# Kernel tuning notes

Measured on AMD Instinct MI355X. Metric: run time of the kernel, lower is better.

Reference implementation:

```python
import jax, jax.numpy as jnp
import numpy as np
import math

PHI = (1 + math.sqrt(5)) / 2
PI = math.pi
B, L, D, V, NL, PAD = 2, 384, 256, 32000, 3, 0


def _ln(t, eps):
    mu = t.mean(-1, keepdims=True)
    var = ((t - mu) ** 2).mean(-1, keepdims=True)
    return (t - mu) / jnp.sqrt(var + eps)


def setup_inputs() -> dict:
    key = jax.random.key(0)
    ks = jax.random.split(key, 8)
    return {
        'x': jax.random.randint(ks[0], (B, L), 0, V, dtype=jnp.int32),
        'emb_real': jax.random.normal(ks[1], (V, D), jnp.float32) * 0.02,
        'emb_imag': jax.random.normal(ks[2], (V, D), jnp.float32) * 0.02,
        'layer_phases': jax.random.normal(ks[3], (NL, D), jnp.float32) * 0.02,
        'interference_weights': jax.random.normal(ks[4], (NL, D), jnp.float32) * 0.02,
        'energy_levels': jnp.linspace(0.0, 1.0, D).astype(jnp.float32),
        'excitation_factor': jnp.ones((1,), jnp.float32) * 0.1,
        'phase_preservation': jnp.ones((NL, D), jnp.float32) * 0.1,
        'coherence_factor': jnp.ones((NL, 1), jnp.float32) * 0.1,
        'W_attn': jax.random.normal(ks[5], (NL, D, D), jnp.float32) * 0.02,
        'out_w': jax.random.normal(ks[6], (2 * D, V), jnp.float32) * 0.02,
        'out_b': jnp.zeros((V,), jnp.float32),
    }


def _forward(x, emb_real, emb_imag, layer_phases, interference_weights,
             energy_levels, excitation_factor, phase_preservation,
             coherence_factor, W_attn, out_w, out_b):
    re = emb_real[x] * 0.1                      # [B,L,D]
    _unused_imag = emb_imag[x] * 0.1            # imag embedding unused downstream (as in original)
    # ---- EnhancedDynamicPhaseSpace ----
    fr = jnp.zeros_like(re)
    fi = jnp.zeros_like(re)
    for i in range(NL):
        pa = jnp.tanh(layer_phases[i]) * PI * PHI      # [D]
        r = _ln(re * jnp.cos(pa), 1e-8)
        im = _ln(re * jnp.sin(pa), 1e-8)
        w = jnp.tanh(interference_weights[i])
        r = r * w
        im = im * w
        a = 2.0 * PI * i / NL
        ca, sa = math.cos(a), math.sin(a)
        fr = fr + r * ca - im * sa
        fi = fi + r * sa + im * ca
    amp = jnp.sqrt(fr * fr + fi * fi + 1e-8)
    coll = (amp < 0.1).astype(re.dtype)
    exc = jnp.exp(energy_levels) * excitation_factor   # [D]
    fr = fr + coll * exc
    fi = fi + coll * exc
    nrm = jnp.sqrt(fr * fr + fi * fi + 1e-8)
    real = jnp.clip(fr / nrm, -1.0, 1.0)
    imag = jnp.clip(fi / nrm, -1.0, 1.0)
    # ---- 3 QuantumStatePreservingAttention layers ----
    pad_mask = (x == PAD)                               # [B,L]
    scale = D ** (-0.5)
    for i in range(NL):
        # q/k/v LayerNorms are parameter-free here and q=k=v, so one norm each
        nr = _ln(real, 1e-5)
        ni = _ln(imag, 1e-5)
        ph = jnp.arctan2(ni + 1e-8, nr + 1e-8)          # [B,L,D]
        pdiff = ph[:, :, None, :] - ph[:, None, :, :]   # [B,L,L,D]
        interf = jnp.cos(pdiff)                         # [B,L,L,D]
        # mean over last dim of (interf @ W) == interf . row-means of W (same math)
        w_mean = W_attn[i].mean(axis=1)                 # [D]
        scores = jnp.einsum('blmd,d->blm', interf, w_mean) * scale
        scores = jnp.where(pad_mask[:, None, :], -jnp.inf, scores)
        attn = jnp.clip(jax.nn.softmax(scores, axis=-1), 1e-6, 1.0)
        out_r = jnp.einsum('blm,bmd->bld', attn, nr)
        out_i = jnp.einsum('blm,bmd->bld', attn, ni)
        coh = interf.mean(axis=(-1, -2))                # [B,L]
        cf = jax.nn.sigmoid(coherence_factor[i]) * coh[..., None]
        phase = jnp.arctan2(out_i + 1e-8, out_r + 1e-8)
        pres = jax.nn.sigmoid(phase_preservation[i]) * cf
        pr = out_r * jnp.cos(phase * pres)
        pim = out_i * jnp.sin(phase * pres)
        real = jnp.clip(_ln(real + 0.01 * pr, 1e-8), -1.0, 1.0)
        _dead = _ln(imag + 0.01 * pim, 1e-8)            # computed then overwritten in original
        imag = real                                     # original bug: imag = clamp(real, -1, 1)
    combined = _ln(jnp.concatenate([real, imag], axis=-1), 1e-5)
    logits = jnp.clip((combined @ out_w + out_b) * 0.1, -10.0, 10.0)
    return logits


def reference(x, emb_real, emb_imag, layer_phases, interference_weights,
              energy_levels, excitation_factor, phase_preservation,
              coherence_factor, W_attn, out_w, out_b):
    return _forward(x, emb_real, emb_imag, layer_phases, interference_weights,
                    energy_levels, excitation_factor, phase_preservation,
                    coherence_factor, W_attn, out_w, out_b)
```

## Files before the change

kernel.cpp:

```cpp
#include <hip/hip_runtime.h>
#include <hip/hip_bf16.h>
#include <math.h>

typedef __hip_bfloat16 bf16;
typedef __bf16 bf16x8 __attribute__((ext_vector_type(8)));
typedef float f32x4 __attribute__((ext_vector_type(4)));

#define NTOK 768
#define SEQ  384
#define DDIM 256
#define VOC  32000

__device__ __forceinline__ float bf2f(bf16 v) { return __bfloat162float(v); }

__device__ __forceinline__ bool probe_bf(const void* energy) {
    return ((const unsigned short*)energy)[1] != 0;
}
__device__ __forceinline__ float ldin(const void* p, long i, bool bf) {
    return bf ? bf2f(((const bf16*)p)[i]) : ((const float*)p)[i];
}

__device__ __forceinline__ float blk_sum256(float v, float* red) {
    #pragma unroll
    for (int o = 32; o > 0; o >>= 1) v += __shfl_down(v, o, 64);
    int w = threadIdx.x >> 6;
    __syncthreads();
    if ((threadIdx.x & 63) == 0) red[w] = v;
    __syncthreads();
    return red[0] + red[1] + red[2] + red[3];
}

__device__ __forceinline__ void np_emit(int t, int d, float nrv, float niv, bool dual,
                                        const float* __restrict__ wm,
                                        float* __restrict__ nrO, float* __restrict__ niO,
                                        float* __restrict__ Co, float* __restrict__ So,
                                        bf16* __restrict__ ASh, bf16* __restrict__ ASl,
                                        bf16* __restrict__ BSh, bf16* __restrict__ BSl)
{
    float ph = atan2f(niv + 1e-8f, nrv + 1e-8f);
    float Cv = cosf(ph), Sv = sinf(ph);
    long idx = (long)t * DDIM + d;
    nrO[idx] = nrv;
    if (dual) niO[idx] = niv;
    Co[idx] = Cv;
    So[idx] = Sv;
    float wv = wm[d];
    float aC = Cv * wv, aS = Sv * wv;
    long o0 = (long)t * 512 + d, o1 = o0 + 256;
    bf16 h;
    h = __float2bfloat16(aC); ASh[o0] = h; ASl[o0] = __float2bfloat16(aC - bf2f(h));
    h = __float2bfloat16(aS); ASh[o1] = h; ASl[o1] = __float2bfloat16(aS - bf2f(h));
    h = __float2bfloat16(Cv); BSh[o0] = h; BSl[o0] = __float2bfloat16(Cv - bf2f(h));
    h = __float2bfloat16(Sv); BSh[o1] = h; BSl[o1] = __float2bfloat16(Sv - bf2f(h));
}

__global__ __launch_bounds__(256)
void phase_kernel(const int* __restrict__ x, const void* __restrict__ emb,
                  const void* __restrict__ lph, const void* __restrict__ iw,
                  const void* __restrict__ energy, const void* __restrict__ excf,
                  const float* __restrict__ wm0,
                  float* __restrict__ realO,
                  float* __restrict__ nrO, float* __restrict__ niO,
                  float* __restrict__ Co, float* __restrict__ So,
                  bf16* __restrict__ ASh, bf16* __restrict__ ASl,
                  bf16* __restrict__ BSh, bf16* __restrict__ BSl)
{
    __shared__ float red[4];
    bool bf = probe_bf(energy);
    int t = blockIdx.x, d = threadIdx.x;
    int tok = x[t];
    float re = ldin(emb, (long)tok * DDIM + d, bf) * 0.1f;
    float fr = 0.f, fi = 0.f;
    const float ca[3] = {1.0f, -0.5f, -0.5f};
    const float sa[3] = {0.0f, 0.86602540378443864676f, -0.86602540378443864676f};
    #pragma unroll
    for (int i = 0; i < 3; ++i) {
        float pa = tanhf(ldin(lph, i * DDIM + d, bf)) * 3.14159265358979323846f;
        pa = pa * 1.61803398874989484820f;
        float vr = re * cosf(pa);
        float vi = re * sinf(pa);
        float mu = blk_sum256(vr, red) * (1.f / 256.f);
        float dv = vr - mu;
        float var = blk_sum256(dv * dv, red) * (1.f / 256.f);
        float r = dv / sqrtf(var + 1e-8f);
        mu = blk_sum256(vi, red) * (1.f / 256.f);
        float di = vi - mu;
        var = blk_sum256(di * di, red) * (1.f / 256.f);
        float im = di / sqrtf(var + 1e-8f);
        float w = tanhf(ldin(iw, i * DDIM + d, bf));
        r *= w; im *= w;
        fr = fr + r * ca[i] - im * sa[i];
        fi = fi + r * sa[i] + im * ca[i];
    }
    float amp = sqrtf(fr * fr + fi * fi + 1e-8f);
    float ex = expf(ldin(energy, d, bf)) * ldin(excf, 0, bf);
    if (amp < 0.1f) { fr += ex; fi += ex; }
    float nrm = sqrtf(fr * fr + fi * fi + 1e-8f);
    float rr = fminf(fmaxf(fr / nrm, -1.f), 1.f);
    float ii = fminf(fmaxf(fi / nrm, -1.f), 1.f);
    realO[t * DDIM + d] = rr;
    float mu = blk_sum256(rr, red) * (1.f / 256.f);
    float dv = rr - mu;
    float var = blk_sum256(dv * dv, red) * (1.f / 256.f);
    float nrv = dv / sqrtf(var + 1e-5f);
    mu = blk_sum256(ii, red) * (1.f / 256.f);
    float di = ii - mu;
    var = blk_sum256(di * di, red) * (1.f / 256.f);
    float niv = di / sqrtf(var + 1e-5f);
    np_emit(t, d, nrv, niv, true, wm0, nrO, niO, Co, So, ASh, ASl, BSh, BSl);
}

__global__ __launch_bounds__(256)
void wmean_kernel(const void* __restrict__ W, const void* __restrict__ energy,
                  float* __restrict__ wmAll)
{
    bool bf = probe_bf(energy);
    int row = blockIdx.x * 4 + (threadIdx.x >> 6);
    int lane = threadIdx.x & 63;
    long base = (long)row * DDIM + lane * 4;
    float s = 0.f;
    #pragma unroll
    for (int j = 0; j < 4; ++j) s += ldin(W, base + j, bf);
    #pragma unroll
    for (int o = 32; o > 0; o >>= 1) s += __shfl_down(s, o, 64);
    if (lane == 0) wmAll[row] = s * (1.f / 256.f) * 0.0625f;
}

__global__ __launch_bounds__(256)
void sums_kernel(const float* __restrict__ C, const float* __restrict__ S,
                 float* __restrict__ Cp, float* __restrict__ Sp)
{
    int c = blockIdx.x, b = blockIdx.y, d = threadIdx.x;
    float cs = 0.f, ss = 0.f;
    int base = (b * SEQ + c * 16) * DDIM + d;
    #pragma unroll
    for (int m = 0; m < 16; ++m) { cs += C[base + m * DDIM]; ss += S[base + m * DDIM]; }
    Cp[(b * 24 + c) * DDIM + d] = cs;
    Sp[(b * 24 + c) * DDIM + d] = ss;
}

__global__ __launch_bounds__(256)
void transpose_kernel(const float* __restrict__ nr, const float* __restrict__ ni,
                      bf16* __restrict__ nrTh, bf16* __restrict__ nrTl,
                      bf16* __restrict__ niTh, bf16* __restrict__ niTl, int dual)
{
    __shared__ float tr[64][65], ti[64][65];
    int m0 = blockIdx.x * 64, d0 = blockIdx.y * 64, b = blockIdx.z;
    int c = threadIdx.x & 63, rr = threadIdx.x >> 6;
    #pragma unroll
    for (int i = 0; i < 16; ++i) {
        int r = i * 4 + rr;
        tr[r][c] = nr[(b * SEQ + m0 + r) * DDIM + d0 + c];
        if (dual) ti[r][c] = ni[(b * SEQ + m0 + r) * DDIM + d0 + c];
    }
    __syncthreads();
    #pragma unroll
    for (int i = 0; i < 16; ++i) {
        int dd = i * 4 + rr;
        long o = (long)(b * DDIM + d0 + dd) * SEQ + m0 + c;
        float vr = tr[c][dd];
        bf16 h;
        h = __float2bfloat16(vr); nrTh[o] = h; nrTl[o] = __float2bfloat16(vr - bf2f(h));
        if (dual) {
            float vi = ti[c][dd];
            h = __float2bfloat16(vi); niTh[o] = h; niTl[o] = __float2bfloat16(vi - bf2f(h));
        }
    }
}

__device__ __forceinline__ void gload_lds16(const bf16* g, bf16* l) {
    __builtin_amdgcn_global_load_lds(
        (const __attribute__((address_space(1))) unsigned int*)g,
        (__attribute__((address_space(3))) unsigned int*)l,
        16, 0, 0);
}

__global__ __launch_bounds__(256, 4)
void scores_mfma(const bf16* __restrict__ ASh, const bf16* __restrict__ ASl,
                 const bf16* __restrict__ BSh, const bf16* __restrict__ BSl,
                 float* __restrict__ scores)
{
    __shared__ bf16 ldsA[2][64 * 64];
    __shared__ bf16 ldsB[2][32 * 64];
    int l0 = blockIdx.x * 64, m0 = blockIdx.y * 32, b = blockIdx.z;
    int tid = threadIdx.x, lane = tid & 63, wid = tid >> 6;
    int wr = wid >> 1, wc = wid & 1;
    int lrow = lane >> 3;
    int cbs  = (lane & 7) ^ lrow;

    const bf16* srcA = (wid == 1 ? ASl : ASh) + (size_t)(b * SEQ + l0) * 512;
    const bf16* srcB = (wid == 3 ? BSl : BSh) + (size_t)(b * SEQ + m0) * 512;

    f32x4 acc[2] = {};

    for (int k0 = 0; k0 < 512; k0 += 64) {
        if (wid < 2) {
            bf16* ld = &ldsA[wid][0];
            #pragma unroll
            for (int q = 0; q < 8; ++q)
                gload_lds16(srcA + (size_t)(q * 8 + lrow) * 512 + k0 + cbs * 8, ld + q * 512);
        } else {
            bf16* ld = &ldsB[wid - 2][0];
            #pragma unroll
            for (int q = 0; q < 4; ++q)
                gload_lds16(srcB + (size_t)(q * 8 + lrow) * 512 + k0 + cbs * 8, ld + q * 512);
        }
        __syncthreads();
        #pragma unroll
        for (int ks = 0; ks < 2; ++ks) {
            int cb = ks * 64 + (lane >> 4) * 16;
            int rowb = wc * 16 + (lane & 15);
            int offb = rowb * 128 + (cb ^ ((rowb & 7) << 4));
            bf16x8 bh = *(const bf16x8*)((const char*)&ldsB[0][0] + offb);
            bf16x8 bl = *(const bf16x8*)((const char*)&ldsB[1][0] + offb);
            #pragma unroll
            for (int fm = 0; fm < 2; ++fm) {
                int rowa = wr * 32 + fm * 16 + (lane & 15);
                int offa = rowa * 128 + (cb ^ ((rowa & 7) << 4));
                bf16x8 ah = *(const bf16x8*)((const char*)&ldsA[0][0] + offa);
                bf16x8 al = *(const bf16x8*)((const char*)&ldsA[1][0] + offa);
                acc[fm] = __builtin_amdgcn_mfma_f32_16x16x32_bf16(ah, bh, acc[fm], 0, 0, 0);
                acc[fm] = __builtin_amdgcn_mfma_f32_16x16x32_bf16(ah, bl, acc[fm], 0, 0, 0);
                acc[fm] = __builtin_amdgcn_mfma_f32_16x16x32_bf16(al, bh, acc[fm], 0, 0, 0);
            }
        }
        __syncthreads();
    }

    int mm = m0 + wc * 16 + (lane & 15);
    #pragma unroll
    for (int fm = 0; fm < 2; ++fm) {
        int lbase = l0 + wr * 32 + fm * 16 + (lane >> 4) * 4;
        #pragma unroll
        for (int i = 0; i < 4; ++i)
            scores[(size_t)(b * SEQ + lbase + i) * SEQ + mm] = acc[fm][i];
    }
}

__global__ __launch_bounds__(384)
void softmax_kernel(const float* __restrict__ scores, const int* __restrict__ x,
                    bf16* __restrict__ Ph, bf16* __restrict__ Pl)
{
    __shared__ float red[6];
    int row = blockIdx.x;
    int b = row / SEQ;
    int m = threadIdx.x;
    float s = scores[row * SEQ + m];
    if (x[b * SEQ + m] == 0) s = -__builtin_inff();
    float v = s;
    #pragma unroll
    for (int o = 32; o > 0; o >>= 1) v = fmaxf(v, __shfl_down(v, o, 64));
    if ((threadIdx.x & 63) == 0) red[threadIdx.x >> 6] = v;
    __syncthreads();
    float mx = red[0];
    #pragma unroll
    for (int i = 1; i < 6; ++i) mx = fmaxf(mx, red[i]);
    float p = expf(s - mx);
    __syncthreads();
    v = p;
    #pragma unroll
    for (int o = 32; o > 0; o >>= 1) v += __shfl_down(v, o, 64);
    if ((threadIdx.x & 63) == 0) red[threadIdx.x >> 6] = v;
    __syncthreads();
    float sum = red[0] + red[1] + red[2] + red[3] + red[4] + red[5];
    float pv = p / sum;
    pv = fminf(fmaxf(pv, 1e-6f), 1.0f);
    bf16 h = __float2bfloat16(pv);
    Ph[(size_t)row * SEQ + m] = h;
    Pl[(size_t)row * SEQ + m] = __float2bfloat16(pv - bf2f(h));
}

__global__ __launch_bounds__(256, 4)
void outgemm_mfma(const bf16* __restrict__ Ph, const bf16* __restrict__ Pl,
                  const bf16* __restrict__ nrTh, const bf16* __restrict__ nrTl,
                  const bf16* __restrict__ niTh, const bf16* __restrict__ niTl,
                  float* __restrict__ outr, float* __restrict__ outi, int dual)
{
    __shared__ bf16 ldsA[2][64 * 64];
    __shared__ bf16 ldsB[4][32 * 64];
    int l0 = blockIdx.x * 64, d0 = blockIdx.y * 32, b = blockIdx.z;
    int tid = threadIdx.x, lane = tid & 63, wid = tid >> 6;
    int wr = wid >> 1, wc = wid & 1;
    int lrow = lane >> 3, cbs = (lane & 7) ^ lrow;

    const bf16* sA  = (wid == 0 ? Ph : Pl) + (size_t)(b * SEQ + l0) * SEQ;
    const bf16* sB1 = (wid == 2 ? nrTh : nrTl) + (size_t)(b * DDIM + d0) * SEQ;
    const bf16* sB2 = (wid == 2 ? niTh : niTl) + (size_t)(b * DDIM + d0) * SEQ;

    f32x4 accr[2] = {}, acci[2] = {};

    for (int k0 = 0; k0 < SEQ; k0 += 64) {
        if (wid < 2) {
            bf16* ld = &ldsA[wid][0];
            #pragma unroll
            for (int q = 0; q < 8; ++q)
                gload_lds16(sA + (size_t)(q * 8 + lrow) * SEQ + k0 + cbs * 8, ld + q * 512);
        } else {
            bf16* l1 = &ldsB[wid - 2][0];
            #pragma unroll
            for (int q = 0; q < 4; ++q)
                gload_lds16(sB1 + (size_t)(q * 8 + lrow) * SEQ + k0 + cbs * 8, l1 + q * 512);
            if (dual) {
                bf16* l2 = &ldsB[wid][0];
                #pragma unroll
                for (int q = 0; q < 4; ++q)
                    gload_lds16(sB2 + (size_t)(q * 8 + lrow) * SEQ + k0 + cbs * 8, l2 + q * 512);
            }
        }
        __syncthreads();
        #pragma unroll
        for (int ks = 0; ks < 2; ++ks) {
            int cb = ks * 64 + (lane >> 4) * 16;
            int rowb = wc * 16 + (lane & 15);
            int offb = rowb * 128 + (cb ^ ((rowb & 7) << 4));
            bf16x8 brh = *(const bf16x8*)((const char*)&ldsB[0][0] + offb);
            bf16x8 brl = *(const bf16x8*)((const char*)&ldsB[1][0] + offb);
            #pragma unroll
            for (int fm = 0; fm < 2; ++fm) {
                int rowa = wr * 32 + fm * 16 + (lane & 15);
                int offa = rowa * 128 + (cb ^ ((rowa & 7) << 4));
                bf16x8 ah = *(const bf16x8*)((const char*)&ldsA[0][0] + offa);
                bf16x8 al = *(const bf16x8*)((const char*)&ldsA[1][0] + offa);
                accr[fm] = __builtin_amdgcn_mfma_f32_16x16x32_bf16(ah, brh, accr[fm], 0, 0, 0);
                accr[fm] = __builtin_amdgcn_mfma_f32_16x16x32_bf16(ah, brl, accr[fm], 0, 0, 0);
                accr[fm] = __builtin_amdgcn_mfma_f32_16x16x32_bf16(al, brh, accr[fm], 0, 0, 0);
            }
            if (dual) {
                bf16x8 bih = *(const bf16x8*)((const char*)&ldsB[2][0] + offb);
                bf16x8 bil = *(const bf16x8*)((const char*)&ldsB[3][0] + offb);
                #pragma unroll
                for (int fm = 0; fm < 2; ++fm) {
                    int rowa = wr * 32 + fm * 16 + (lane & 15);
                    int offa = rowa * 128 + (cb ^ ((rowa & 7) << 4));
                    bf16x8 ah = *(const bf16x8*)((const char*)&ldsA[0][0] + offa);
                    bf16x8 al = *(const bf16x8*)((const char*)&ldsA[1][0] + offa);
                    acci[fm] = __builtin_amdgcn_mfma_f32_16x16x32_bf16(ah, bih, acci[fm], 0, 0, 0);
                    acci[fm] = __builtin_amdgcn_mfma_f32_16x16x32_bf16(ah, bil, acci[fm], 0, 0, 0);
                    acci[fm] = __builtin_amdgcn_mfma_f32_16x16x32_bf16(al, bih, acci[fm], 0, 0, 0);
                }
            }
        }
        __syncthreads();
    }

    int d = d0 + wc * 16 + (lane & 15);
    #pragma unroll
    for (int fm = 0; fm < 2; ++fm) {
        int lb = l0 + wr * 32 + fm * 16 + (lane >> 4) * 4;
        #pragma unroll
        for (int i = 0; i < 4; ++i) {
            size_t idx = (size_t)(b * SEQ + lb + i) * DDIM + d;
            outr[idx] = accr[fm][i];
            if (dual) outi[idx] = acci[fm][i];
        }
    }
}

__global__ __launch_bounds__(256)
void update_kernel(float* __restrict__ realA,
                   const float* __restrict__ outr, const float* __restrict__ outi,
                   const float* __restrict__ C, const float* __restrict__ S,
                   const float* __restrict__ Cp, const float* __restrict__ Sp,
                   const void* __restrict__ pp, const void* __restrict__ cfac,
                   const void* __restrict__ energy, int layer, int mode,
                   const float* __restrict__ wmNext,
                   float* __restrict__ nrO, float* __restrict__ Co, float* __restrict__ So,
                   bf16* __restrict__ ASh, bf16* __restrict__ ASl,
                   bf16* __restrict__ BSh, bf16* __restrict__ BSl,
                   bf16* __restrict__ Ah, bf16* __restrict__ Al)
{
    __shared__ float red[4];
    bool bf = probe_bf(energy);
    int t = blockIdx.x, d = threadIdx.x;
    int b = t / SEQ;
    long idx = (long)t * DDIM + d;
    float cs = 0.f, ss = 0.f;
    #pragma unroll
    for (int c = 0; c < 24; ++c) {
        cs += Cp[(b * 24 + c) * DDIM + d];
        ss += Sp[(b * 24 + c) * DDIM + d];
    }
    float dotv = C[idx] * cs + S[idx] * ss;
    float coh = blk_sum256(dotv, red) * (1.0f / (384.f * 256.f));
    float cf = (1.f / (1.f + expf(-ldin(cfac, layer, bf)))) * coh;
    float orr = outr[idx], oii = outi[idx];
    float phase = atan2f(oii + 1e-8f, orr + 1e-8f);
    float pres = (1.f / (1.f + expf(-ldin(pp, layer * DDIM + d, bf)))) * cf;
    float pr = orr * cosf(phase * pres);
    float v = realA[idx] + 0.01f * pr;
    float mu = blk_sum256(v, red) * (1.f / 256.f);
    float dv = v - mu;
    float var = blk_sum256(dv * dv, red) * (1.f / 256.f);
    float nv = dv / sqrtf(var + 1e-8f);
    nv = fminf(fmaxf(nv, -1.f), 1.f);
    realA[idx] = nv;
    float mu2 = blk_sum256(nv, red) * (1.f / 256.f);
    float dv2 = nv - mu2;
    float var2 = blk_sum256(dv2 * dv2, red) * (1.f / 256.f);
    float nn = dv2 / sqrtf(var2 + 1e-5f);
    if (mode == 0) {
        np_emit(t, d, nn, nn, false, wmNext, nrO, nullptr, Co, So, ASh, ASl, BSh, BSl);
    } else {
        bf16 h = __float2bfloat16(nn);
        Ah[idx] = h;
        Al[idx] = __float2bfloat16(nn - bf2f(h));
    }
}


__global__ __launch_bounds__(256)
void fold_kernel(const void* __restrict__ W, const void* __restrict__ energy,
                 bf16* __restrict__ Bh, bf16* __restrict__ Bl)
{
    __shared__ float tile[64][65];
    bool bf = probe_bf(energy);
    int v0 = blockIdx.x * 64, d0 = blockIdx.y * 64;
    int c = threadIdx.x & 63, rr = threadIdx.x >> 6;
    #pragma unroll
    for (int i = 0; i < 16; ++i) {
        int r = i * 4 + rr;
        long i1 = (long)(d0 + r) * VOC + v0 + c;
        long i2 = (long)(d0 + r + 256) * VOC + v0 + c;
        tile[r][c] = ldin(W, i1, bf) + ldin(W, i2, bf);
    }
    __syncthreads();
    int d = threadIdx.x & 63, vv = threadIdx.x >> 6;
    #pragma unroll
    for (int i = 0; i < 16; ++i) {
        int v = i * 4 + vv;
        float s = tile[d][v];
        bf16 h = __float2bfloat16(s);
        long o = (long)(v0 + v) * DDIM + d0 + d;
        Bh[o] = h;
        Bl[o] = __float2bfloat16(s - __bfloat162float(h));
    }
}

__global__ __launch_bounds__(512, 4)
void vocab_gemm(const bf16* __restrict__ Ah, const bf16* __restrict__ Al,
                const bf16* __restrict__ Bh, const bf16* __restrict__ Bl,
                const void* __restrict__ bias, const void* __restrict__ energy,
                void* __restrict__ out)
{
    __shared__ bf16 lds[4][128 * 64];
    bool bf = probe_bf(energy);
    int flat = blockIdx.x + blockIdx.y * 6;
    int xcd = flat & 7, bidx = flat >> 3;
    int swz = (xcd < 4) ? xcd * 188 + bidx : 752 + (xcd - 4) * 187 + bidx;
    int m0 = (swz % 6) * 128, n0 = (swz / 6) * 128;
    int tid = threadIdx.x, lane = tid & 63, wid = tid >> 6;
    int wm = wid >> 2, wn = wid & 3;
    int arr = wid >> 1, half = wid & 1;

    const bf16* src;
    if      (arr == 0) src = Ah + (size_t)m0 * DDIM;
    else if (arr == 1) src = Al + (size_t)m0 * DDIM;
    else if (arr == 2) src = Bh + (size_t)n0 * DDIM;
    else               src = Bl + (size_t)n0 * DDIM;
    src += (size_t)half * 64 * DDIM;
    bf16* ldst = &lds[arr][half * 64 * 64];
    int lrow = lane >> 3;
    int cbs  = (lane & 7) ^ lrow;

    f32x4 acc[4][2] = {};

    for (int k0 = 0; k0 < DDIM; k0 += 64) {
        #pragma unroll
        for (int q = 0; q < 8; ++q) {
            const bf16* g = src + (size_t)(q * 8 + lrow) * DDIM + k0 + cbs * 8;
            gload_lds16(g, ldst + q * 512);
        }
        __syncthreads();

        #pragma unroll
        for (int ks = 0; ks < 2; ++ks) {
            int cb = ks * 64 + (lane >> 4) * 16;
            bf16x8 bhf[2], blf[2];
            #pragma unroll
            for (int fn = 0; fn < 2; ++fn) {
                int row = wn * 32 + fn * 16 + (lane & 15);
                int off = row * 128 + (cb ^ ((row & 7) << 4));
                bhf[fn] = *(const bf16x8*)((const char*)&lds[2][0] + off);
                blf[fn] = *(const bf16x8*)((const char*)&lds[3][0] + off);
            }
            #pragma unroll
            for (int fm = 0; fm < 4; ++fm) {
                int row = wm * 64 + fm * 16 + (lane & 15);
                int off = row * 128 + (cb ^ ((row & 7) << 4));
                bf16x8 ah = *(const bf16x8*)((const char*)&lds[0][0] + off);
                bf16x8 al = *(const bf16x8*)((const char*)&lds[1][0] + off);
                #pragma unroll
                for (int fn = 0; fn < 2; ++fn) {
                    acc[fm][fn] = __builtin_amdgcn_mfma_f32_16x16x32_bf16(ah, bhf[fn], acc[fm][fn], 0, 0, 0);
                    acc[fm][fn] = __builtin_amdgcn_mfma_f32_16x16x32_bf16(ah, blf[fn], acc[fm][fn], 0, 0, 0);
                    acc[fm][fn] = __builtin_amdgcn_mfma_f32_16x16x32_bf16(al, bhf[fn], acc[fm][fn], 0, 0, 0);
                }
            }
        }
        __syncthreads();
    }

    #pragma unroll
    for (int fn = 0; fn < 2; ++fn) {
        int n = n0 + wn * 32 + fn * 16 + (lane & 15);
        float bv = ldin(bias, n, bf);
        #pragma unroll
        for (int fm = 0; fm < 4; ++fm) {
            int mbase = m0 + wm * 64 + fm * 16 + (lane >> 4) * 4;
            #pragma unroll
            for (int i = 0; i < 4; ++i) {
                float lg = (acc[fm][fn][i] + bv) * 0.1f;
                lg = fminf(fmaxf(lg, -10.f), 10.f);
                size_t idx = (size_t)(mbase + i) * VOC + n;
                if (bf) ((bf16*)out)[idx] = __float2bfloat16(lg);
                else    ((float*)out)[idx] = lg;
            }
        }
    }
}

extern "C" void kernel_launch(void* const* d_in, const int* in_sizes, int n_in,
                              void* d_out, int out_size, void* d_ws, size_t ws_size,
                              hipStream_t stream) {
    (void)in_sizes; (void)n_in; (void)out_size; (void)ws_size;
    const int*  x        = (const int*)d_in[0];
    const void* emb_real = d_in[1];
    const void* lph      = d_in[3];
    const void* iw       = d_in[4];
    const void* energy   = d_in[5];
    const void* excf     = d_in[6];
    const void* pp       = d_in[7];
    const void* cfac     = d_in[8];
    const void* Wattn    = d_in[9];
    const void* out_w    = d_in[10];
    const void* out_b    = d_in[11];

    float* ws = (float*)d_ws;
    const int TD = NTOK * DDIM;
    float* realA = ws;
    float* nr    = realA + TD;
    float* ni    = nr + TD;
    float* Cc    = ni + TD;
    float* Ss    = Cc + TD;
    float* outr  = Ss + TD;
    float* outi  = outr + TD;
    float* attn  = outi + TD;
    float* Cp    = attn + 2 * SEQ * SEQ;
    float* Sp    = Cp + 48 * DDIM;
    float* wmAll = Sp + 48 * DDIM;
    bf16* Ah  = (bf16*)(wmAll + 768);
    bf16* Al  = Ah + (size_t)NTOK * DDIM;
    bf16* Wth = Al + (size_t)NTOK * DDIM;
    bf16* Wtl = Wth + (size_t)VOC * DDIM;
    bf16* ASh = Wtl + (size_t)VOC * DDIM;
    bf16* ASl = ASh + (size_t)NTOK * 512;
    bf16* BSh = ASl + (size_t)NTOK * 512;
    bf16* BSl = BSh + (size_t)NTOK * 512;
    bf16* Phb = BSl + (size_t)NTOK * 512;
    bf16* Plb = Phb + (size_t)NTOK * SEQ;
    bf16* nrTh = Plb + (size_t)NTOK * SEQ;
    bf16* nrTl = nrTh + (size_t)NTOK * DDIM;
    bf16* niTh = nrTl + (size_t)NTOK * DDIM;
    bf16* niTl = niTh + (size_t)NTOK * DDIM;

    fold_kernel<<<dim3(VOC / 64, DDIM / 64), 256, 0, stream>>>(out_w, energy, Wth, Wtl);
    wmean_kernel<<<192, 256, 0, stream>>>(Wattn, energy, wmAll);

    phase_kernel<<<NTOK, 256, 0, stream>>>(x, emb_real, lph, iw, energy, excf, wmAll,
                                           realA, nr, ni, Cc, Ss, ASh, ASl, BSh, BSl);
    for (int layer = 0; layer < 3; ++layer) {
        int dual = (layer == 0);
        sums_kernel<<<dim3(24, 2), 256, 0, stream>>>(Cc, Ss, Cp, Sp);
        transpose_kernel<<<dim3(6, 4, 2), 256, 0, stream>>>(nr, ni, nrTh, nrTl, niTh, niTl, dual);
        scores_mfma<<<dim3(6, 12, 2), 256, 0, stream>>>(ASh, ASl, BSh, BSl, attn);
        softmax_kernel<<<NTOK, 384, 0, stream>>>(attn, x, Phb, Plb);
        outgemm_mfma<<<dim3(6, 8, 2), 256, 0, stream>>>(Phb, Plb, nrTh, nrTl, niTh, niTl,
                                                        outr, outi, dual);
        update_kernel<<<NTOK, 256, 0, stream>>>(realA, outr, dual ? outi : outr, Cc, Ss,
                                                Cp, Sp, pp, cfac, energy, layer,
                                                (layer < 2) ? 0 : 1,
                                                wmAll + (layer + 1 < 3 ? (layer + 1) * DDIM : 0),
                                                nr, Cc, Ss, ASh, ASl, BSh, BSl, Ah, Al);
    }
    vocab_gemm<<<dim3(6, VOC / 128), 512, 0, stream>>>(Ah, Al, Wth, Wtl, out_b, energy, (void*)d_out);
}
```

Before: 367.7 us.

## Fuse per-layer attention kernels into one cooperative persistent kernel with grid syncs

Replaces the 18 per-layer kernel launches (sums, transpose, scores, softmax, outgemm, update) with a single cooperative kernel. It walks work units in a grid-stride loop and separates the phases with grid-wide syncs. Scores and outgemm tiles shrink to 32x32 per block so more blocks share the work, and sums/transpose/scores run in the same phase. The goal is to remove launch overhead and inter-kernel gaps. The cost is grid-sync latency and smaller tiles with less reuse, and the old multi-kernel path stays as a fallback if the cooperative launch fails.

```diff
diff --git a/kernel.cpp b/kernel.cpp
--- a/kernel.cpp
+++ b/kernel.cpp
@@ -1,4 +1,5 @@
 #include <hip/hip_runtime.h>
+#include <hip/hip_cooperative_groups.h>
 #include <hip/hip_bf16.h>
 #include <math.h>
 
@@ -20,14 +21,21 @@
     return bf ? bf2f(((const bf16*)p)[i]) : ((const float*)p)[i];
 }
 
-__device__ __forceinline__ float blk_sum256(float v, float* red) {
+__device__ __forceinline__ float blk_sum256s(float v, float* red) {
     #pragma unroll
     for (int o = 32; o > 0; o >>= 1) v += __shfl_down(v, o, 64);
-    int w = threadIdx.x >> 6;
     __syncthreads();
-    if ((threadIdx.x & 63) == 0) red[w] = v;
+    if ((threadIdx.x & 63) == 0) red[threadIdx.x >> 6] = v;
     __syncthreads();
     return red[0] + red[1] + red[2] + red[3];
+}
+__device__ __forceinline__ float blk_max256s(float v, float* red) {
+    #pragma unroll
+    for (int o = 32; o > 0; o >>= 1) v = fmaxf(v, __shfl_down(v, o, 64));
+    __syncthreads();
+    if ((threadIdx.x & 63) == 0) red[threadIdx.x >> 6] = v;
+    __syncthreads();
+    return fmaxf(fmaxf(red[0], red[1]), fmaxf(red[2], red[3]));
 }
 
 __device__ __forceinline__ void np_emit(int t, int d, float nrv, float niv, bool dual,
@@ -54,6 +62,349 @@
     h = __float2bfloat16(Sv); BSh[o1] = h; BSl[o1] = __float2bfloat16(Sv - bf2f(h));
 }
 
+__device__ __forceinline__ void gload_lds16(const bf16* g, bf16* l) {
+    __builtin_amdgcn_global_load_lds(
+        (const __attribute__((address_space(1))) unsigned int*)g,
+        (__attribute__((address_space(3))) unsigned int*)l,
+        16, 0, 0);
+}
+
+
+__device__ __forceinline__ void scores_unit(int l0, int m0, int b, char* smem,
+    const bf16* __restrict__ ASh, const bf16* __restrict__ ASl,
+    const bf16* __restrict__ BSh, const bf16* __restrict__ BSl,
+    float* __restrict__ scores)
+{
+    bf16* ldsA0 = (bf16*)smem;
+    bf16* ldsA1 = ldsA0 + 2048;
+    bf16* ldsB0 = ldsA1 + 2048;
+    bf16* ldsB1 = ldsB0 + 2048;
+    int tid = threadIdx.x, lane = tid & 63, wid = tid >> 6;
+    int wr = wid >> 1, wc = wid & 1;
+    int lrow = lane >> 3, cbs = (lane & 7) ^ lrow;
+    const bf16* src = (wid == 0 ? ASh : wid == 1 ? ASl : wid == 2 ? BSh : BSl)
+                      + (size_t)(b * SEQ + (wid < 2 ? l0 : m0)) * 512;
+    bf16* ld = (wid == 0 ? ldsA0 : wid == 1 ? ldsA1 : wid == 2 ? ldsB0 : ldsB1);
+    f32x4 acc = {};
+    for (int k0 = 0; k0 < 512; k0 += 64) {
+        #pragma unroll
+        for (int q = 0; q < 4; ++q)
+            gload_lds16(src + (size_t)(q * 8 + lrow) * 512 + k0 + cbs * 8, ld + q * 512);
+        __syncthreads();
+        #pragma unroll
+        for (int ks = 0; ks < 2; ++ks) {
+            int cb = ks * 64 + (lane >> 4) * 16;
+            int rowb = wc * 16 + (lane & 15);
+            int offb = rowb * 128 + (cb ^ ((rowb & 7) << 4));
+            bf16x8 bh = *(const bf16x8*)((const char*)ldsB0 + offb);
+            bf16x8 bl = *(const bf16x8*)((const char*)ldsB1 + offb);
+            int rowa = wr * 16 + (lane & 15);
+            int offa = rowa * 128 + (cb ^ ((rowa & 7) << 4));
+            bf16x8 ah = *(const bf16x8*)((const char*)ldsA0 + offa);
+            bf16x8 al = *(const bf16x8*)((const char*)ldsA1 + offa);
+            acc = __builtin_amdgcn_mfma_f32_16x16x32_bf16(ah, bh, acc, 0, 0, 0);
+            acc = __builtin_amdgcn_mfma_f32_16x16x32_bf16(ah, bl, acc, 0, 0, 0);
+            acc = __builtin_amdgcn_mfma_f32_16x16x32_bf16(al, bh, acc, 0, 0, 0);
+        }
+        __syncthreads();
+    }
+    int mm = m0 + wc * 16 + (lane & 15);
+    int lbase = l0 + wr * 16 + (lane >> 4) * 4;
+    #pragma unroll
+    for (int i = 0; i < 4; ++i)
+        scores[(size_t)(b * SEQ + lbase + i) * SEQ + mm] = acc[i];
+}
+
+__device__ __forceinline__ void transpose_unit(int m0, int d0, int b, char* smem, int dual,
+    const float* __restrict__ nr, const float* __restrict__ ni,
+    bf16* __restrict__ nrTh, bf16* __restrict__ nrTl,
+    bf16* __restrict__ niTh, bf16* __restrict__ niTl)
+{
+    float* tr = (float*)smem;
+    float* ti = tr + 64 * 65;
+    int c = threadIdx.x & 63, rr = threadIdx.x >> 6;
+    #pragma unroll
+    for (int i = 0; i < 16; ++i) {
+        int r = i * 4 + rr;
+        tr[r * 65 + c] = nr[(b * SEQ + m0 + r) * DDIM + d0 + c];
+        if (dual) ti[r * 65 + c] = ni[(b * SEQ + m0 + r) * DDIM + d0 + c];
+    }
+    __syncthreads();
+    #pragma unroll
+    for (int i = 0; i < 16; ++i) {
+        int dd = i * 4 + rr;
+        long o = (long)(b * DDIM + d0 + dd) * SEQ + m0 + c;
+        float vr = tr[c * 65 + dd];
+        bf16 h;
+        h = __float2bfloat16(vr); nrTh[o] = h; nrTl[o] = __float2bfloat16(vr - bf2f(h));
+        if (dual) {
+            float vi = ti[c * 65 + dd];
+            h = __float2bfloat16(vi); niTh[o] = h; niTl[o] = __float2bfloat16(vi - bf2f(h));
+        }
+    }
+    __syncthreads();
+}
+
+__device__ __forceinline__ void sums_unit(int c, int b,
+    const float* __restrict__ C, const float* __restrict__ S,
+    float* __restrict__ Cp, float* __restrict__ Sp)
+{
+    int d = threadIdx.x;
+    float cs = 0.f, ss = 0.f;
+    int base = (b * SEQ + c * 16) * DDIM + d;
+    #pragma unroll
+    for (int m = 0; m < 16; ++m) { cs += C[base + m * DDIM]; ss += S[base + m * DDIM]; }
+    Cp[(b * 24 + c) * DDIM + d] = cs;
+    Sp[(b * 24 + c) * DDIM + d] = ss;
+}
+
+__device__ __forceinline__ void softmax_unit(int row, float* red,
+    const float* __restrict__ scores, const int* __restrict__ x,
+    bf16* __restrict__ Ph, bf16* __restrict__ Pl)
+{
+    int b = row / SEQ;
+    int tid = threadIdx.x;
+    float s1 = scores[(size_t)row * SEQ + tid];
+    if (x[b * SEQ + tid] == 0) s1 = -__builtin_inff();
+    float s2 = -__builtin_inff();
+    if (tid < 128) {
+        s2 = scores[(size_t)row * SEQ + 256 + tid];
+        if (x[b * SEQ + 256 + tid] == 0) s2 = -__builtin_inff();
+    }
+    float mx = blk_max256s(fmaxf(s1, s2), red);
+    float e1 = expf(s1 - mx);
+    float e2 = (tid < 128) ? expf(s2 - mx) : 0.f;
+    float sum = blk_sum256s(e1 + e2, red);
+    float p1 = fminf(fmaxf(e1 / sum, 1e-6f), 1.0f);
+    bf16 h = __float2bfloat16(p1);
+    Ph[(size_t)row * SEQ + tid] = h;
+    Pl[(size_t)row * SEQ + tid] = __float2bfloat16(p1 - bf2f(h));
+    if (tid < 128) {
+        float p2 = fminf(fmaxf(e2 / sum, 1e-6f), 1.0f);
+        h = __float2bfloat16(p2);
+        Ph[(size_t)row * SEQ + 256 + tid] = h;
+        Pl[(size_t)row * SEQ + 256 + tid] = __float2bfloat16(p2 - bf2f(h));
+    }
+}
+
+__device__ __forceinline__ void outgemm_unit(int l0, int d0, int b, char* smem, int dual,
+    const bf16* __restrict__ Ph, const bf16* __restrict__ Pl,
+    const bf16* __restrict__ nrTh, const bf16* __restrict__ nrTl,
+    const bf16* __restrict__ niTh, const bf16* __restrict__ niTl,
+    float* __restrict__ outr, float* __restrict__ outi)
+{
+    bf16* ldsA0 = (bf16*)smem;
+    bf16* ldsA1 = ldsA0 + 2048;
+    bf16* ldsB0 = ldsA1 + 2048;
+    bf16* ldsB1 = ldsB0 + 2048;
+    bf16* ldsB2 = ldsB1 + 2048;
+    bf16* ldsB3 = ldsB2 + 2048;
+    int tid = threadIdx.x, lane = tid & 63, wid = tid >> 6;
+    int wr = wid >> 1, wc = wid & 1;
+    int lrow = lane >> 3, cbs = (lane & 7) ^ lrow;
+
+    const bf16* sA  = (wid == 0 ? Ph : Pl) + (size_t)(b * SEQ + l0) * SEQ;
+    const bf16* sB1 = (wid == 2 ? nrTh : nrTl) + (size_t)(b * DDIM + d0) * SEQ;
+    const bf16* sB2 = (wid == 2 ? niTh : niTl) + (size_t)(b * DDIM + d0) * SEQ;
+
+    f32x4 accr = {}, acci = {};
+
+    for (int k0 = 0; k0 < SEQ; k0 += 64) {
+        if (wid < 2) {
+            bf16* ld = (wid == 0) ? ldsA0 : ldsA1;
+            #pragma unroll
+            for (int q = 0; q < 4; ++q)
+                gload_lds16(sA + (size_t)(q * 8 + lrow) * SEQ + k0 + cbs * 8, ld + q * 512);
+        } else {
+            bf16* l1 = (wid == 2) ? ldsB0 : ldsB1;
+            #pragma unroll
+            for (int q = 0; q < 4; ++q)
+                gload_lds16(sB1 + (size_t)(q * 8 + lrow) * SEQ + k0 + cbs * 8, l1 + q * 512);
+            if (dual) {
+                bf16* l2 = (wid == 2) ? ldsB2 : ldsB3;
+                #pragma unroll
+                for (int q = 0; q < 4; ++q)
+                    gload_lds16(sB2 + (size_t)(q * 8 + lrow) * SEQ + k0 + cbs * 8, l2 + q * 512);
+            }
+        }
+        __syncthreads();
+        #pragma unroll
+        for (int ks = 0; ks < 2; ++ks) {
+            int cb = ks * 64 + (lane >> 4) * 16;
+            int rowb = wc * 16 + (lane & 15);
+            int offb = rowb * 128 + (cb ^ ((rowb & 7) << 4));
+            int rowa = wr * 16 + (lane & 15);
+            int offa = rowa * 128 + (cb ^ ((rowa & 7) << 4));
+            bf16x8 ah = *(const bf16x8*)((const char*)ldsA0 + offa);
+            bf16x8 al = *(const bf16x8*)((const char*)ldsA1 + offa);
+            bf16x8 brh = *(const bf16x8*)((const char*)ldsB0 + offb);
+            bf16x8 brl = *(const bf16x8*)((const char*)ldsB1 + offb);
+            accr = __builtin_amdgcn_mfma_f32_16x16x32_bf16(ah, brh, accr, 0, 0, 0);
+            accr = __builtin_amdgcn_mfma_f32_16x16x32_bf16(ah, brl, accr, 0, 0, 0);
+            accr = __builtin_amdgcn_mfma_f32_16x16x32_bf16(al, brh, accr, 0, 0, 0);
+            if (dual) {
+                bf16x8 bih = *(const bf16x8*)((const char*)ldsB2 + offb);
+                bf16x8 bil = *(const bf16x8*)((const char*)ldsB3 + offb);
+                acci = __builtin_amdgcn_mfma_f32_16x16x32_bf16(ah, bih, acci, 0, 0, 0);
+                acci = __builtin_amdgcn_mfma_f32_16x16x32_bf16(ah, bil, acci, 0, 0, 0);
+                acci = __builtin_amdgcn_mfma_f32_16x16x32_bf16(al, bih, acci, 0, 0, 0);
+            }
+        }
+        __syncthreads();
+    }
+
+    int d = d0 + wc * 16 + (lane & 15);
+    int lb = l0 + wr * 16 + (lane >> 4) * 4;
+    #pragma unroll
+    for (int i = 0; i < 4; ++i) {
+        size_t idx = (size_t)(b * SEQ + lb + i) * DDIM + d;
+        outr[idx] = accr[i];
+        if (dual) outi[idx] = acci[i];
+    }
+}
+
+__device__ __forceinline__ void update_unit(int t, float* red,
+    float* __restrict__ realA,
+    const float* __restrict__ outr, const float* __restrict__ outi,
+    const float* __restrict__ C, const float* __restrict__ S,
+    const float* __restrict__ Cp, const float* __restrict__ Sp,
+    const void* __restrict__ pp, const void* __restrict__ cfac,
+    const void* __restrict__ energy, int layer, int mode,
+    const float* __restrict__ wmNext,
+    float* __restrict__ nrO, float* __restrict__ Co, float* __restrict__ So,
+    bf16* __restrict__ ASh, bf16* __restrict__ ASl,
+    bf16* __restrict__ BSh, bf16* __restrict__ BSl,
+    bf16* __restrict__ Ah, bf16* __restrict__ Al)
+{
+    bool bf = probe_bf(energy);
+    int d = threadIdx.x;
+    int b = t / SEQ;
+    long idx = (long)t * DDIM + d;
+    float cs = 0.f, ss = 0.f;
+    #pragma unroll
+    for (int c = 0; c < 24; ++c) {
+        cs += Cp[(b * 24 + c) * DDIM + d];
+        ss += Sp[(b * 24 + c) * DDIM + d];
+    }
+    float dotv = C[idx] * cs + S[idx] * ss;
+    float coh = blk_sum256s(dotv, red) * (1.0f / (384.f * 256.f));
+    float cf = (1.f / (1.f + expf(-ldin(cfac, layer, bf)))) * coh;
+    float orr = outr[idx], oii = outi[idx];
+    float phase = atan2f(oii + 1e-8f, orr + 1e-8f);
+    float pres = (1.f / (1.f + expf(-ldin(pp, layer * DDIM + d, bf)))) * cf;
+    float pr = orr * cosf(phase * pres);
+    float v = realA[idx] + 0.01f * pr;
+    float mu = blk_sum256s(v, red) * (1.f / 256.f);
+    float dv = v - mu;
+    float var = blk_sum256s(dv * dv, red) * (1.f / 256.f);
+    float nv = dv / sqrtf(var + 1e-8f);
+    nv = fminf(fmaxf(nv, -1.f), 1.f);
+    realA[idx] = nv;
+    float mu2 = blk_sum256s(nv, red) * (1.f / 256.f);
+    float dv2 = nv - mu2;
+    float var2 = blk_sum256s(dv2 * dv2, red) * (1.f / 256.f);
+    float nn = dv2 / sqrtf(var2 + 1e-5f);
+    if (mode == 0) {
+        np_emit(t, d, nn, nn, false, wmNext, nrO, nullptr, Co, So, ASh, ASl, BSh, BSl);
+    } else {
+        bf16 h = __float2bfloat16(nn);
+        Ah[idx] = h;
+        Al[idx] = __float2bfloat16(nn - bf2f(h));
+    }
+}
+
+struct CoopArgs {
+    const int* x;
+    const void* pp; const void* cfac; const void* energy;
+    float* realA; float* nr; float* ni; float* Cc; float* Ss;
+    float* outr; float* outi; float* attn; float* Cp; float* Sp;
+    const float* wmAll;
+    bf16 *ASh, *ASl, *BSh, *BSl, *Phb, *Plb;
+    bf16 *nrTh, *nrTl, *niTh, *niTl, *Ah, *Al;
+};
+
+__global__ __launch_bounds__(256)
+void coop_layers(CoopArgs a)
+{
+    __shared__ __align__(16) char smem[33280];
+    cooperative_groups::grid_group g = cooperative_groups::this_grid();
+    int bid = blockIdx.x, G = gridDim.x;
+    for (int layer = 0; layer < 3; ++layer) {
+        int dual = (layer == 0);
+        for (int u = bid; u < 384; u += G) {
+            if (u < 288)
+                scores_unit((u % 12) * 32, ((u / 12) % 12) * 32, u / 144, smem,
+                            a.ASh, a.ASl, a.BSh, a.BSl, a.attn);
+            else if (u < 336) {
+                int v = u - 288;
+                transpose_unit((v % 6) * 64, ((v / 6) % 4) * 64, v / 24, smem, dual,
+                               a.nr, a.ni, a.nrTh, a.nrTl, a.niTh, a.niTl);
+            } else {
+                int w = u - 336;
+                sums_unit(w % 24, w / 24, a.Cc, a.Ss, a.Cp, a.Sp);
+            }
+        }
+        g.sync();
+        for (int row = bid; row < NTOK; row += G)
+            softmax_unit(row, (float*)smem, a.attn, a.x, a.Phb, a.Plb);
+        g.sync();
+        for (int u = bid; u < 192; u += G)
+            outgemm_unit((u % 12) * 32, ((u / 12) % 8) * 32, u / 96, smem, dual,
+                         a.Phb, a.Plb, a.nrTh, a.nrTl, a.niTh, a.niTl, a.outr, a.outi);
+        g.sync();
+        int mode = (layer < 2) ? 0 : 1;
+        const float* wmN = a.wmAll + ((layer + 1 < 3) ? (layer + 1) * DDIM : 0);
+        for (int t = bid; t < NTOK; t += G)
+            update_unit(t, (float*)smem, a.realA, a.outr, dual ? a.outi : a.outr,
+                        a.Cc, a.Ss, a.Cp, a.Sp, a.pp, a.cfac, a.energy, layer, mode, wmN,
+                        a.nr, a.Cc, a.Ss, a.ASh, a.ASl, a.BSh, a.BSl, a.Ah, a.Al);
+        g.sync();
+    }
+}
+
+__global__ __launch_bounds__(256)
+void scores_k(const bf16* ASh, const bf16* ASl, const bf16* BSh, const bf16* BSl, float* scores)
+{
+    __shared__ __align__(16) char smem[16384];
+    scores_unit(blockIdx.x * 32, blockIdx.y * 32, blockIdx.z, smem, ASh, ASl, BSh, BSl, scores);
+}
+__global__ __launch_bounds__(256)
+void transpose_k(const float* nr, const float* ni, bf16* nrTh, bf16* nrTl,
+                 bf16* niTh, bf16* niTl, int dual)
+{
+    __shared__ __align__(16) char smem[33280];
+    transpose_unit(blockIdx.x * 64, blockIdx.y * 64, blockIdx.z, smem, dual,
+                   nr, ni, nrTh, nrTl, niTh, niTl);
+}
+__global__ __launch_bounds__(256)
+void sums_k(const float* C, const float* S, float* Cp, float* Sp)
+{ sums_unit(blockIdx.x, blockIdx.y, C, S, Cp, Sp); }
+__global__ __launch_bounds__(256)
+void softmax_k(const float* scores, const int* x, bf16* Ph, bf16* Pl)
+{
+    __shared__ float red[4];
+    softmax_unit(blockIdx.x, red, scores, x, Ph, Pl);
+}
+__global__ __launch_bounds__(256)
+void outgemm_k(const bf16* Ph, const bf16* Pl, const bf16* nrTh, const bf16* nrTl,
+               const bf16* niTh, const bf16* niTl, float* outr, float* outi, int dual)
+{
+    __shared__ __align__(16) char smem[24576];
+    outgemm_unit(blockIdx.x * 32, blockIdx.y * 32, blockIdx.z, smem, dual,
+                 Ph, Pl, nrTh, nrTl, niTh, niTl, outr, outi);
+}
+__global__ __launch_bounds__(256)
+void update_k(float* realA, const float* outr, const float* outi,
+              const float* C, const float* S, const float* Cp, const float* Sp,
+              const void* pp, const void* cfac, const void* energy, int layer, int mode,
+              const float* wmNext, float* nrO, float* Co, float* So,
+              bf16* ASh, bf16* ASl, bf16* BSh, bf16* BSl, bf16* Ah, bf16* Al)
+{
+    __shared__ float red[4];
+    update_unit(blockIdx.x, red, realA, outr, outi, C, S, Cp, Sp, pp, cfac, energy,
+                layer, mode, wmNext, nrO, Co, So, ASh, ASl, BSh, BSl, Ah, Al);
+}
+
 __global__ __launch_bounds__(256)
 void phase_kernel(const int* __restrict__ x, const void* __restrict__ emb,
                   const void* __restrict__ lph, const void* __restrict__ iw,
@@ -79,13 +430,13 @@
         pa = pa * 1.61803398874989484820f;
         float vr = re * cosf(pa);
         float vi = re * sinf(pa);
-        float mu = blk_sum256(vr, red) * (1.f / 256.f);
+        float mu = blk_sum256s(vr, red) * (1.f / 256.f);
         float dv = vr - mu;
-        float var = blk_sum256(dv * dv, red) * (1.f / 256.f);
+        float var = blk_sum256s(dv * dv, red) * (1.f / 256.f);
         float r = dv / sqrtf(var + 1e-8f);
-        mu = blk_sum256(vi, red) * (1.f / 256.f);
+        mu = blk_sum256s(vi, red) * (1.f / 256.f);
         float di = vi - mu;
-        var = blk_sum256(di * di, red) * (1.f / 256.f);
+        var = blk_sum256s(di * di, red) * (1.f / 256.f);
         float im = di / sqrtf(var + 1e-8f);
         float w = tanhf(ldin(iw, i * DDIM + d, bf));
         r *= w; im *= w;
@@ -99,13 +450,13 @@
     float rr = fminf(fmaxf(fr / nrm, -1.f), 1.f);
     float ii = fminf(fmaxf(fi / nrm, -1.f), 1.f);
     realO[t * DDIM + d] = rr;
-    float mu = blk_sum256(rr, red) * (1.f / 256.f);
+    float mu = blk_sum256s(rr, red) * (1.f / 256.f);
     float dv = rr - mu;
-    float var = blk_sum256(dv * dv, red) * (1.f / 256.f);
+    float var = blk_sum256s(dv * dv, red) * (1.f / 256.f);
     float nrv = dv / sqrtf(var + 1e-5f);
-    mu = blk_sum256(ii, red) * (1.f / 256.f);
+    mu = blk_sum256s(ii, red) * (1.f / 256.f);
     float di = ii - mu;
-    var = blk_sum256(di * di, red) * (1.f / 256.f);
+    var = blk_sum256s(di * di, red) * (1.f / 256.f);
     float niv = di / sqrtf(var + 1e-5f);
     np_emit(t, d, nrv, niv, true, wm0, nrO, niO, Co, So, ASh, ASl, BSh, BSl);
 }
@@ -125,288 +476,6 @@
     for (int o = 32; o > 0; o >>= 1) s += __shfl_down(s, o, 64);
     if (lane == 0) wmAll[row] = s * (1.f / 256.f) * 0.0625f;
 }
-
-__global__ __launch_bounds__(256)
-void sums_kernel(const float* __restrict__ C, const float* __restrict__ S,
-                 float* __restrict__ Cp, float* __restrict__ Sp)
-{
-    int c = blockIdx.x, b = blockIdx.y, d = threadIdx.x;
-    float cs = 0.f, ss = 0.f;
-    int base = (b * SEQ + c * 16) * DDIM + d;
-    #pragma unroll
-    for (int m = 0; m < 16; ++m) { cs += C[base + m * DDIM]; ss += S[base + m * DDIM]; }
-    Cp[(b * 24 + c) * DDIM + d] = cs;
-    Sp[(b * 24 + c) * DDIM + d] = ss;
-}
-
-__global__ __launch_bounds__(256)
-void transpose_kernel(const float* __restrict__ nr, const float* __restrict__ ni,
-                      bf16* __restrict__ nrTh, bf16* __restrict__ nrTl,
-                      bf16* __restrict__ niTh, bf16* __restrict__ niTl, int dual)
-{
-    __shared__ float tr[64][65], ti[64][65];
-    int m0 = blockIdx.x * 64, d0 = blockIdx.y * 64, b = blockIdx.z;
-    int c = threadIdx.x & 63, rr = threadIdx.x >> 6;
-    #pragma unroll
-    for (int i = 0; i < 16; ++i) {
-        int r = i * 4 + rr;
-        tr[r][c] = nr[(b * SEQ + m0 + r) * DDIM + d0 + c];
-        if (dual) ti[r][c] = ni[(b * SEQ + m0 + r) * DDIM + d0 + c];
-    }
-    __syncthreads();
-    #pragma unroll
-    for (int i = 0; i < 16; ++i) {
-        int dd = i * 4 + rr;
-        long o = (long)(b * DDIM + d0 + dd) * SEQ + m0 + c;
-        float vr = tr[c][dd];
-        bf16 h;
-        h = __float2bfloat16(vr); nrTh[o] = h; nrTl[o] = __float2bfloat16(vr - bf2f(h));
-        if (dual) {
-            float vi = ti[c][dd];
-            h = __float2bfloat16(vi); niTh[o] = h; niTl[o] = __float2bfloat16(vi - bf2f(h));
-        }
-    }
-}
-
-__device__ __forceinline__ void gload_lds16(const bf16* g, bf16* l) {
-    __builtin_amdgcn_global_load_lds(
-        (const __attribute__((address_space(1))) unsigned int*)g,
-        (__attribute__((address_space(3))) unsigned int*)l,
-        16, 0, 0);
-}
-
-__global__ __launch_bounds__(256, 4)
-void scores_mfma(const bf16* __restrict__ ASh, const bf16* __restrict__ ASl,
-                 const bf16* __restrict__ BSh, const bf16* __restrict__ BSl,
-                 float* __restrict__ scores)
-{
-    __shared__ bf16 ldsA[2][64 * 64];
-    __shared__ bf16 ldsB[2][32 * 64];
-    int l0 = blockIdx.x * 64, m0 = blockIdx.y * 32, b = blockIdx.z;
-    int tid = threadIdx.x, lane = tid & 63, wid = tid >> 6;
-    int wr = wid >> 1, wc = wid & 1;
-    int lrow = lane >> 3;
-    int cbs  = (lane & 7) ^ lrow;
-
-    const bf16* srcA = (wid == 1 ? ASl : ASh) + (size_t)(b * SEQ + l0) * 512;
-    const bf16* srcB = (wid == 3 ? BSl : BSh) + (size_t)(b * SEQ + m0) * 512;
-
-    f32x4 acc[2] = {};
-
-    for (int k0 = 0; k0 < 512; k0 += 64) {
-        if (wid < 2) {
-            bf16* ld = &ldsA[wid][0];
-            #pragma unroll
-            for (int q = 0; q < 8; ++q)
-                gload_lds16(srcA + (size_t)(q * 8 + lrow) * 512 + k0 + cbs * 8, ld + q * 512);
-        } else {
-            bf16* ld = &ldsB[wid - 2][0];
-            #pragma unroll
-            for (int q = 0; q < 4; ++q)
-                gload_lds16(srcB + (size_t)(q * 8 + lrow) * 512 + k0 + cbs * 8, ld + q * 512);
-        }
-        __syncthreads();
-        #pragma unroll
-        for (int ks = 0; ks < 2; ++ks) {
-            int cb = ks * 64 + (lane >> 4) * 16;
-            int rowb = wc * 16 + (lane & 15);
-            int offb = rowb * 128 + (cb ^ ((rowb & 7) << 4));
-            bf16x8 bh = *(const bf16x8*)((const char*)&ldsB[0][0] + offb);
-            bf16x8 bl = *(const bf16x8*)((const char*)&ldsB[1][0] + offb);
-            #pragma unroll
-            for (int fm = 0; fm < 2; ++fm) {
-                int rowa = wr * 32 + fm * 16 + (lane & 15);
-                int offa = rowa * 128 + (cb ^ ((rowa & 7) << 4));
-                bf16x8 ah = *(const bf16x8*)((const char*)&ldsA[0][0] + offa);
-                bf16x8 al = *(const bf16x8*)((const char*)&ldsA[1][0] + offa);
-                acc[fm] = __builtin_amdgcn_mfma_f32_16x16x32_bf16(ah, bh, acc[fm], 0, 0, 0);
-                acc[fm] = __builtin_amdgcn_mfma_f32_16x16x32_bf16(ah, bl, acc[fm], 0, 0, 0);
-                acc[fm] = __builtin_amdgcn_mfma_f32_16x16x32_bf16(al, bh, acc[fm], 0, 0, 0);
-            }
-        }
-        __syncthreads();
-    }
-
-    int mm = m0 + wc * 16 + (lane & 15);
-    #pragma unroll
-    for (int fm = 0; fm < 2; ++fm) {
-        int lbase = l0 + wr * 32 + fm * 16 + (lane >> 4) * 4;
-        #pragma unroll
-        for (int i = 0; i < 4; ++i)
-            scores[(size_t)(b * SEQ + lbase + i) * SEQ + mm] = acc[fm][i];
-    }
-}
-
-__global__ __launch_bounds__(384)
-void softmax_kernel(const float* __restrict__ scores, const int* __restrict__ x,
-                    bf16* __restrict__ Ph, bf16* __restrict__ Pl)
-{
-    __shared__ float red[6];
-    int row = blockIdx.x;
-    int b = row / SEQ;
-    int m = threadIdx.x;
-    float s = scores[row * SEQ + m];
-    if (x[b * SEQ + m] == 0) s = -__builtin_inff();
-    float v = s;
-    #pragma unroll
-    for (int o = 32; o > 0; o >>= 1) v = fmaxf(v, __shfl_down(v, o, 64));
-    if ((threadIdx.x & 63) == 0) red[threadIdx.x >> 6] = v;
-    __syncthreads();
-    float mx = red[0];
-    #pragma unroll
-    for (int i = 1; i < 6; ++i) mx = fmaxf(mx, red[i]);
-    float p = expf(s - mx);
-    __syncthreads();
-    v = p;
-    #pragma unroll
-    for (int o = 32; o > 0; o >>= 1) v += __shfl_down(v, o, 64);
-    if ((threadIdx.x & 63) == 0) red[threadIdx.x >> 6] = v;
-    __syncthreads();
-    float sum = red[0] + red[1] + red[2] + red[3] + red[4] + red[5];
-    float pv = p / sum;
-    pv = fminf(fmaxf(pv, 1e-6f), 1.0f);
-    bf16 h = __float2bfloat16(pv);
-    Ph[(size_t)row * SEQ + m] = h;
-    Pl[(size_t)row * SEQ + m] = __float2bfloat16(pv - bf2f(h));
-}
-
-__global__ __launch_bounds__(256, 4)
-void outgemm_mfma(const bf16* __restrict__ Ph, const bf16* __restrict__ Pl,
-                  const bf16* __restrict__ nrTh, const bf16* __restrict__ nrTl,
-                  const bf16* __restrict__ niTh, const bf16* __restrict__ niTl,
-                  float* __restrict__ outr, float* __restrict__ outi, int dual)
-{
-    __shared__ bf16 ldsA[2][64 * 64];
-    __shared__ bf16 ldsB[4][32 * 64];
-    int l0 = blockIdx.x * 64, d0 = blockIdx.y * 32, b = blockIdx.z;
-    int tid = threadIdx.x, lane = tid & 63, wid = tid >> 6;
-    int wr = wid >> 1, wc = wid & 1;
-    int lrow = lane >> 3, cbs = (lane & 7) ^ lrow;
-
-    const bf16* sA  = (wid == 0 ? Ph : Pl) + (size_t)(b * SEQ + l0) * SEQ;
-    const bf16* sB1 = (wid == 2 ? nrTh : nrTl) + (size_t)(b * DDIM + d0) * SEQ;
-    const bf16* sB2 = (wid == 2 ? niTh : niTl) + (size_t)(b * DDIM + d0) * SEQ;
-
-    f32x4 accr[2] = {}, acci[2] = {};
-
-    for (int k0 = 0; k0 < SEQ; k0 += 64) {
-        if (wid < 2) {
-            bf16* ld = &ldsA[wid][0];
-            #pragma unroll
-            for (int q = 0; q < 8; ++q)
-                gload_lds16(sA + (size_t)(q * 8 + lrow) * SEQ + k0 + cbs * 8, ld + q * 512);
-        } else {
-            bf16* l1 = &ldsB[wid - 2][0];
-            #pragma unroll
-            for (int q = 0; q < 4; ++q)
-                gload_lds16(sB1 + (size_t)(q * 8 + lrow) * SEQ + k0 + cbs * 8, l1 + q * 512);
-            if (dual) {
-                bf16* l2 = &ldsB[wid][0];
-                #pragma unroll
-                for (int q = 0; q < 4; ++q)
-                    gload_lds16(sB2 + (size_t)(q * 8 + lrow) * SEQ + k0 + cbs * 8, l2 + q * 512);
-            }
-        }
-        __syncthreads();
-        #pragma unroll
-        for (int ks = 0; ks < 2; ++ks) {
-            int cb = ks * 64 + (lane >> 4) * 16;
-            int rowb = wc * 16 + (lane & 15);
-            int offb = rowb * 128 + (cb ^ ((rowb & 7) << 4));
-            bf16x8 brh = *(const bf16x8*)((const char*)&ldsB[0][0] + offb);
-            bf16x8 brl = *(const bf16x8*)((const char*)&ldsB[1][0] + offb);
-            #pragma unroll
-            for (int fm = 0; fm < 2; ++fm) {
-                int rowa = wr * 32 + fm * 16 + (lane & 15);
-                int offa = rowa * 128 + (cb ^ ((rowa & 7) << 4));
-                bf16x8 ah = *(const bf16x8*)((const char*)&ldsA[0][0] + offa);
-                bf16x8 al = *(const bf16x8*)((const char*)&ldsA[1][0] + offa);
-                accr[fm] = __builtin_amdgcn_mfma_f32_16x16x32_bf16(ah, brh, accr[fm], 0, 0, 0);
-                accr[fm] = __builtin_amdgcn_mfma_f32_16x16x32_bf16(ah, brl, accr[fm], 0, 0, 0);
-                accr[fm] = __builtin_amdgcn_mfma_f32_16x16x32_bf16(al, brh, accr[fm], 0, 0, 0);
-            }
-            if (dual) {
-                bf16x8 bih = *(const bf16x8*)((const char*)&ldsB[2][0] + offb);
-                bf16x8 bil = *(const bf16x8*)((const char*)&ldsB[3][0] + offb);
-                #pragma unroll
-                for (int fm = 0; fm < 2; ++fm) {
-                    int rowa = wr * 32 + fm * 16 + (lane & 15);
-                    int offa = rowa * 128 + (cb ^ ((rowa & 7) << 4));
-                    bf16x8 ah = *(const bf16x8*)((const char*)&ldsA[0][0] + offa);
-                    bf16x8 al = *(const bf16x8*)((const char*)&ldsA[1][0] + offa);
-                    acci[fm] = __builtin_amdgcn_mfma_f32_16x16x32_bf16(ah, bih, acci[fm], 0, 0, 0);
-                    acci[fm] = __builtin_amdgcn_mfma_f32_16x16x32_bf16(ah, bil, acci[fm], 0, 0, 0);
-                    acci[fm] = __builtin_amdgcn_mfma_f32_16x16x32_bf16(al, bih, acci[fm], 0, 0, 0);
-                }
-            }
-        }
-        __syncthreads();
-    }
-
-    int d = d0 + wc * 16 + (lane & 15);
-    #pragma unroll
-    for (int fm = 0; fm < 2; ++fm) {
-        int lb = l0 + wr * 32 + fm * 16 + (lane >> 4) * 4;
-        #pragma unroll
-        for (int i = 0; i < 4; ++i) {
-            size_t idx = (size_t)(b * SEQ + lb + i) * DDIM + d;
-            outr[idx] = accr[fm][i];
-            if (dual) outi[idx] = acci[fm][i];
-        }
-    }
-}
-
-__global__ __launch_bounds__(256)
-void update_kernel(float* __restrict__ realA,
-                   const float* __restrict__ outr, const float* __restrict__ outi,
-                   const float* __restrict__ C, const float* __restrict__ S,
-                   const float* __restrict__ Cp, const float* __restrict__ Sp,
-                   const void* __restrict__ pp, const void* __restrict__ cfac,
-                   const void* __restrict__ energy, int layer, int mode,
-                   const float* __restrict__ wmNext,
-                   float* __restrict__ nrO, float* __restrict__ Co, float* __restrict__ So,
-                   bf16* __restrict__ ASh, bf16* __restrict__ ASl,
-                   bf16* __restrict__ BSh, bf16* __restrict__ BSl,
-                   bf16* __restrict__ Ah, bf16* __restrict__ Al)
-{
-    __shared__ float red[4];
-    bool bf = probe_bf(energy);
-    int t = blockIdx.x, d = threadIdx.x;
-    int b = t / SEQ;
-    long idx = (long)t * DDIM + d;
-    float cs = 0.f, ss = 0.f;
-    #pragma unroll
-    for (int c = 0; c < 24; ++c) {
-        cs += Cp[(b * 24 + c) * DDIM + d];
-        ss += Sp[(b * 24 + c) * DDIM + d];
-    }
-    float dotv = C[idx] * cs + S[idx] * ss;
-    float coh = blk_sum256(dotv, red) * (1.0f / (384.f * 256.f));
-    float cf = (1.f / (1.f + expf(-ldin(cfac, layer, bf)))) * coh;
-    float orr = outr[idx], oii = outi[idx];
-    float phase = atan2f(oii + 1e-8f, orr + 1e-8f);
-    float pres = (1.f / (1.f + expf(-ldin(pp, layer * DDIM + d, bf)))) * cf;
-    float pr = orr * cosf(phase * pres);
-    float v = realA[idx] + 0.01f * pr;
-    float mu = blk_sum256(v, red) * (1.f / 256.f);
-    float dv = v - mu;
-    float var = blk_sum256(dv * dv, red) * (1.f / 256.f);
-    float nv = dv / sqrtf(var + 1e-8f);
-    nv = fminf(fmaxf(nv, -1.f), 1.f);
-    realA[idx] = nv;
-    float mu2 = blk_sum256(nv, red) * (1.f / 256.f);
-    float dv2 = nv - mu2;
-    float var2 = blk_sum256(dv2 * dv2, red) * (1.f / 256.f);
-    float nn = dv2 / sqrtf(var2 + 1e-5f);
-    if (mode == 0) {
-        np_emit(t, d, nn, nn, false, wmNext, nrO, nullptr, Co, So, ASh, ASl, BSh, BSl);
-    } else {
-        bf16 h = __float2bfloat16(nn);
-        Ah[idx] = h;
-        Al[idx] = __float2bfloat16(nn - bf2f(h));
-    }
-}
-
 
 __global__ __launch_bounds__(256)
 void fold_kernel(const void* __restrict__ W, const void* __restrict__ energy,
@@ -467,11 +536,10 @@
     for (int k0 = 0; k0 < DDIM; k0 += 64) {
         #pragma unroll
         for (int q = 0; q < 8; ++q) {
-            const bf16* g = src + (size_t)(q * 8 + lrow) * DDIM + k0 + cbs * 8;
-            gload_lds16(g, ldst + q * 512);
+            const bf16* gp = src + (size_t)(q * 8 + lrow) * DDIM + k0 + cbs * 8;
+            gload_lds16(gp, ldst + q * 512);
         }
         __syncthreads();
-
         #pragma unroll
         for (int ks = 0; ks < 2; ++ks) {
             int cb = ks * 64 + (lane >> 4) * 16;
@@ -565,22 +633,56 @@
 
     fold_kernel<<<dim3(VOC / 64, DDIM / 64), 256, 0, stream>>>(out_w, energy, Wth, Wtl);
     wmean_kernel<<<192, 256, 0, stream>>>(Wattn, energy, wmAll);
-
     phase_kernel<<<NTOK, 256, 0, stream>>>(x, emb_real, lph, iw, energy, excf, wmAll,
                                            realA, nr, ni, Cc, Ss, ASh, ASl, BSh, BSl);
-    for (int layer = 0; layer < 3; ++layer) {
-        int dual = (layer == 0);
-        sums_kernel<<<dim3(24, 2), 256, 0, stream>>>(Cc, Ss, Cp, Sp);
-        transpose_kernel<<<dim3(6, 4, 2), 256, 0, stream>>>(nr, ni, nrTh, nrTl, niTh, niTl, dual);
-        scores_mfma<<<dim3(6, 12, 2), 256, 0, stream>>>(ASh, ASl, BSh, BSl, attn);
-        softmax_kernel<<<NTOK, 384, 0, stream>>>(attn, x, Phb, Plb);
-        outgemm_mfma<<<dim3(6, 8, 2), 256, 0, stream>>>(Phb, Plb, nrTh, nrTl, niTh, niTl,
-                                                        outr, outi, dual);
-        update_kernel<<<NTOK, 256, 0, stream>>>(realA, outr, dual ? outi : outr, Cc, Ss,
-                                                Cp, Sp, pp, cfac, energy, layer,
-                                                (layer < 2) ? 0 : 1,
-                                                wmAll + (layer + 1 < 3 ? (layer + 1) * DDIM : 0),
-                                                nr, Cc, Ss, ASh, ASl, BSh, BSl, Ah, Al);
+
+    static int coop_grid = -2;
+    if (coop_grid == -2) {
+        int dev = 0, nb = 0, ncu = 0;
+        hipGetDevice(&dev);
+        hipDeviceProp_t prop;
+        if (hipGetDeviceProperties(&prop, dev) == hipSuccess) ncu = prop.multiProcessorCount;
+        if (ncu <= 0) ncu = 256;
+        if (hipOccupancyMaxActiveBlocksPerMultiprocessor(&nb, (const void*)coop_layers, 256, 0)
+                != hipSuccess || nb < 1)
+            coop_grid = -1;
+        else {
+            long gsz = (long)nb * ncu;
+            coop_grid = (int)(gsz < 768 ? gsz : 768);
+        }
+    }
+
+    bool did_coop = false;
+    if (coop_grid > 0) {
+        CoopArgs ca;
+        ca.x = x; ca.pp = pp; ca.cfac = cfac; ca.energy = energy;
+        ca.realA = realA; ca.nr = nr; ca.ni = ni; ca.Cc = Cc; ca.Ss = Ss;
+        ca.outr = outr; ca.outi = outi; ca.attn = attn; ca.Cp = Cp; ca.Sp = Sp;
+        ca.wmAll = wmAll;
+        ca.ASh = ASh; ca.ASl = ASl; ca.BSh = BSh; ca.BSl = BSl;
+        ca.Phb = Phb; ca.Plb = Plb;
+        ca.nrTh = nrTh; ca.nrTl = nrTl; ca.niTh = niTh; ca.niTl = niTl;
+        ca.Ah = Ah; ca.Al = Al;
+        void* params[] = { &ca };
+        if (hipLaunchCooperativeKernel((const void*)coop_layers, dim3(coop_grid), dim3(256),
+                                       params, 0, stream) == hipSuccess)
+            did_coop = true;
+    }
+    if (!did_coop) {
+        for (int layer = 0; layer < 3; ++layer) {
+            int dual = (layer == 0);
+            sums_k<<<dim3(24, 2), 256, 0, stream>>>(Cc, Ss, Cp, Sp);
+            transpose_k<<<dim3(6, 4, 2), 256, 0, stream>>>(nr, ni, nrTh, nrTl, niTh, niTl, dual);
+            scores_k<<<dim3(12, 12, 2), 256, 0, stream>>>(ASh, ASl, BSh, BSl, attn);
+            softmax_k<<<NTOK, 256, 0, stream>>>(attn, x, Phb, Plb);
+            outgemm_k<<<dim3(12, 8, 2), 256, 0, stream>>>(Phb, Plb, nrTh, nrTl, niTh, niTl,
+                                                          outr, outi, dual);
+            update_k<<<NTOK, 256, 0, stream>>>(realA, outr, dual ? outi : outr, Cc, Ss,
+                                               Cp, Sp, pp, cfac, energy, layer,
+                                               (layer < 2) ? 0 : 1,
+                                               wmAll + (layer + 1 < 3 ? (layer + 1) * DDIM : 0),
+                                               nr, Cc, Ss, ASh, ASl, BSh, BSl, Ah, Al);
+        }
     }
     vocab_gemm<<<dim3(6, VOC / 128), 512, 0, stream>>>(Ah, Al, Wth, Wtl, out_b, energy, (void*)d_out);
 }
```

After: 757.0 us. +105.8%, slower.
